# Optimization experiments

Hardware: AMD Instinct MI355X
Metric: run time of the kernel (lower is better)

The kernel has to match this reference:

```python
import jax, jax.numpy as jnp
import numpy as np

N = 16384
D_IN = 128
D_OUT = 128
BETA = 1.0


def setup_inputs() -> dict:
    key = jax.random.key(0)
    k1, k2, k3 = jax.random.split(key, 3)
    x = jax.random.normal(k1, (N, D_IN), dtype=jnp.float32)
    adj = jax.random.uniform(k2, (N, N), dtype=jnp.float32)
    # single-layer MLP (mlp_layers=1 -> channels=[in_dim, out_dim] -> one Linear)
    W_mlp = jax.random.normal(k3, (D_IN, D_OUT), dtype=jnp.float32) * (1.0 / np.sqrt(D_IN))
    b_mlp = jnp.zeros((D_OUT,), dtype=jnp.float32)
    return {"x": x, "adj": adj, "W_mlp": W_mlp, "b_mlp": b_mlp}


def reference(x, adj, W_mlp, b_mlp):
    # softmax aggregator: attention = softmax(adj * beta, axis=-1); x = attention @ x
    attention = jax.nn.softmax(adj * BETA, axis=-1)  # [N, N]
    h = jnp.matmul(attention, x)                      # [N, D_IN]
    # MLP with a single linear layer
    out = jnp.matmul(h, W_mlp) + b_mlp                # [N, D_OUT]
    return out
```

## Files before the change

### kernel.cpp

```cpp
#include <hip/hip_runtime.h>
#include <hip/hip_bf16.h>


typedef short  short8  __attribute__((ext_vector_type(8)));
typedef short  short4v __attribute__((ext_vector_type(4)));
typedef float  floatx4 __attribute__((ext_vector_type(4)));

#define NN 16384
#define DD 128

__device__ __forceinline__ short f2bf(float f) {
    unsigned u = __float_as_uint(f);
    u += 0x7fff + ((u >> 16) & 1);
    return (short)(u >> 16);
}

__global__ __launch_bounds__(256, 2) void xw_kernel(
    const float* __restrict__ x, const float* __restrict__ W, short* __restrict__ yT)
{
    __shared__ short WT[128 * 136];
    const int t  = threadIdx.x;
    const int j0 = blockIdx.x * 64;

    #pragma unroll
    for (int i = 0; i < 16; ++i) {
        int f4 = t + 256 * i;
        int d = f4 >> 5, c4 = f4 & 31;
        float4 v = ((const float4*)W)[f4];
        WT[(4*c4 + 0) * 136 + d] = f2bf(v.x);
        WT[(4*c4 + 1) * 136 + d] = f2bf(v.y);
        WT[(4*c4 + 2) * 136 + d] = f2bf(v.z);
        WT[(4*c4 + 3) * 136 + d] = f2bf(v.w);
    }
    __syncthreads();

    const int lane = t & 63, w = t >> 6;
    const int nl = lane & 15, q = lane >> 4;
    const int j = j0 + 16 * w + nl;
    const float* xrow = x + (size_t)j * DD + 8 * q;

    floatx4 acc[8];
    #pragma unroll
    for (int kt = 0; kt < 8; ++kt) acc[kt] = (floatx4){0.f, 0.f, 0.f, 0.f};

    #pragma unroll
    for (int dstep = 0; dstep < 4; ++dstep) {
        float4 v0 = *(const float4*)(xrow + 32 * dstep);
        float4 v1 = *(const float4*)(xrow + 32 * dstep + 4);
        short8 bf;
        bf[0] = f2bf(v0.x); bf[1] = f2bf(v0.y); bf[2] = f2bf(v0.z); bf[3] = f2bf(v0.w);
        bf[4] = f2bf(v1.x); bf[5] = f2bf(v1.y); bf[6] = f2bf(v1.z); bf[7] = f2bf(v1.w);
        #pragma unroll
        for (int kt = 0; kt < 8; ++kt) {
            short8 af = *(const short8*)(&WT[(16*kt + nl) * 136 + 32*dstep + 8*q]);
            acc[kt] = __builtin_amdgcn_mfma_f32_16x16x32_bf16(af, bf, acc[kt], 0, 0, 0);
        }
    }
    #pragma unroll
    for (int kt = 0; kt < 8; ++kt) {
        #pragma unroll
        for (int r = 0; r < 4; ++r)
            yT[(size_t)(16*kt + 4*q + r) * NN + j] = f2bf(acc[kt][r]);
    }
}

__global__ __launch_bounds__(256, 1) void attn_kernel(
    const float* __restrict__ adj, const short* __restrict__ yT,
    const float* __restrict__ bias, float* __restrict__ out)
{
    __shared__ short A_lds[64 * 136];
    __shared__ short B_lds[128 * 136];
    __shared__ float rs[64];

    const int t  = threadIdx.x;
    const int i0 = blockIdx.x * 64;

    const int cg = t & 31, rg = t >> 5;
    const float* aptr = adj + (size_t)(i0 + rg) * NN + 4 * cg;
    const int bn = t >> 1, bh = t & 1;
    const short* bptr = yT + (size_t)bn * NN + 64 * bh;

    float4 pa[8];
    uint4  pb[8];
    float  psum[8];
    floatx4 acc[8];
    #pragma unroll
    for (int p = 0; p < 8; ++p) psum[p] = 0.f;
    #pragma unroll
    for (int n = 0; n < 8; ++n) acc[n] = (floatx4){0.f, 0.f, 0.f, 0.f};

    const int lane = t & 63, w = t >> 6;
    const int m = lane & 15, q = lane >> 4;
    const short* Arow = &A_lds[(16*w + m) * 136];

    auto load_tile = [&](int kb) {
        #pragma unroll
        for (int p = 0; p < 8; ++p)
            pa[p] = *(const float4*)(aptr + (size_t)(8 * p) * NN + kb);
        #pragma unroll
        for (int jj = 0; jj < 8; ++jj)
            pb[jj] = *(const uint4*)(bptr + kb + 8 * jj);
    };
    auto store_tile = [&]() {
        #pragma unroll
        for (int p = 0; p < 8; ++p) {
            float e0 = __expf(pa[p].x), e1 = __expf(pa[p].y);
            float e2 = __expf(pa[p].z), e3 = __expf(pa[p].w);
            psum[p] += (e0 + e1) + (e2 + e3);
            short4v v; v[0] = f2bf(e0); v[1] = f2bf(e1); v[2] = f2bf(e2); v[3] = f2bf(e3);
            *(short4v*)&A_lds[(rg + 8*p) * 136 + 4*cg] = v;
        }
        #pragma unroll
        for (int jj = 0; jj < 8; ++jj)
            *(uint4*)&B_lds[bn * 136 + 64*bh + 8*jj] = pb[jj];
    };
    auto mma_tile = [&]() {
        #pragma unroll
        for (int ks = 0; ks < 4; ++ks) {
            short8 af = *(const short8*)(Arow + 32*ks + 8*q);
            #pragma unroll
            for (int nt = 0; nt < 8; ++nt) {
                short8 bf = *(const short8*)(&B_lds[(16*nt + m) * 136 + 32*ks + 8*q]);
                acc[nt] = __builtin_amdgcn_mfma_f32_16x16x32_bf16(af, bf, acc[nt], 0, 0, 0);
            }
        }
    };

    load_tile(0);
    store_tile();
    __syncthreads();
    for (int it = 1; it < NN / 128; ++it) {
        load_tile(it * 128);
        mma_tile();
        __syncthreads();
        store_tile();
        __syncthreads();
    }
    mma_tile();

    #pragma unroll
    for (int p = 0; p < 8; ++p) {
        float v = psum[p];
        v += __shfl_xor(v, 1);
        v += __shfl_xor(v, 2);
        v += __shfl_xor(v, 4);
        v += __shfl_xor(v, 8);
        v += __shfl_xor(v, 16);
        if (cg == 0) rs[rg + 8*p] = v;
    }
    __syncthreads();

    float inv[4];
    #pragma unroll
    for (int r = 0; r < 4; ++r) inv[r] = 1.0f / rs[16*w + 4*q + r];
    #pragma unroll
    for (int nt = 0; nt < 8; ++nt) {
        float bv = bias[16*nt + m];
        #pragma unroll
        for (int r = 0; r < 4; ++r)
            out[(size_t)(i0 + 16*w + 4*q + r) * DD + 16*nt + m] = acc[nt][r] * inv[r] + bv;
    }
}

extern "C" void kernel_launch(void* const* d_in, const int* in_sizes, int n_in,
                              void* d_out, int out_size, void* d_ws, size_t ws_size,
                              hipStream_t stream)
{
    const float* x    = (const float*)d_in[0];
    const float* adj  = (const float*)d_in[1];
    const float* W    = (const float*)d_in[2];
    const float* bias = (const float*)d_in[3];
    float* out = (float*)d_out;
    short* yT  = (short*)d_ws;

    hipLaunchKernelGGL(xw_kernel,   dim3(256), dim3(256), 0, stream, x, W, yT);
    hipLaunchKernelGGL(attn_kernel, dim3(256), dim3(256), 0, stream, adj, yT, bias, out);
}
```

Baseline: 1.856 ms.

## Load MFMA operands directly from global into registers, dropping LDS staging

The attention kernel no longer stages the exp(adj) tile and the yT tile through shared memory. Each wave now loads its own 16 rows of adj and all of yT straight into registers in MFMA fragment layout, and double-buffers the loads across two register slots, so all __syncthreads barriers go away. Row sums are reduced with lane shuffles. The trade-off is that every wave re-reads the full yT from global/L2, four times per block instead of once, and the loads are scattered 16-byte accesses, not coalesced tile loads.

```diff
diff --git a/kernel.cpp b/kernel.cpp
--- a/kernel.cpp
+++ b/kernel.cpp
@@ -3,7 +3,6 @@
 
 
 typedef short  short8  __attribute__((ext_vector_type(8)));
-typedef short  short4v __attribute__((ext_vector_type(4)));
 typedef float  floatx4 __attribute__((ext_vector_type(4)));
 
 #define NN 16384
@@ -68,97 +67,69 @@
     const float* __restrict__ adj, const short* __restrict__ yT,
     const float* __restrict__ bias, float* __restrict__ out)
 {
-    __shared__ short A_lds[64 * 136];
-    __shared__ short B_lds[128 * 136];
-    __shared__ float rs[64];
+    const int t  = threadIdx.x;
+    const int la = t & 63, w = t >> 6;
+    const int m = la & 15, q = la >> 4;
+    const int i0 = blockIdx.x * 64 + 16 * w;
 
-    const int t  = threadIdx.x;
-    const int i0 = blockIdx.x * 64;
+    const float* aptr = adj + (size_t)(i0 + m) * NN + 8 * q;
+    const short* bptr = yT + (size_t)m * NN + 8 * q;
 
-    const int cg = t & 31, rg = t >> 5;
-    const float* aptr = adj + (size_t)(i0 + rg) * NN + 4 * cg;
-    const int bn = t >> 1, bh = t & 1;
-    const short* bptr = yT + (size_t)bn * NN + 64 * bh;
-
-    float4 pa[8];
-    uint4  pb[8];
-    float  psum[8];
     floatx4 acc[8];
     #pragma unroll
-    for (int p = 0; p < 8; ++p) psum[p] = 0.f;
-    #pragma unroll
-    for (int n = 0; n < 8; ++n) acc[n] = (floatx4){0.f, 0.f, 0.f, 0.f};
+    for (int nt = 0; nt < 8; ++nt) acc[nt] = (floatx4){0.f, 0.f, 0.f, 0.f};
+    float psumA = 0.f, psumB = 0.f;
 
-    const int lane = t & 63, w = t >> 6;
-    const int m = lane & 15, q = lane >> 4;
-    const short* Arow = &A_lds[(16*w + m) * 136];
+    float4 A00, A01, A10, A11;
+    uint4  B0[8], B1[8];
 
-    auto load_tile = [&](int kb) {
+    auto load_slot = [&](int s, float4& Aa, float4& Ab, uint4* B) {
+        const float* ap = aptr + (size_t)s * 32;
+        Aa = *(const float4*)ap;
+        Ab = *(const float4*)(ap + 4);
+        const short* bp = bptr + (size_t)s * 32;
         #pragma unroll
-        for (int p = 0; p < 8; ++p)
-            pa[p] = *(const float4*)(aptr + (size_t)(8 * p) * NN + kb);
+        for (int nt = 0; nt < 8; ++nt)
+            B[nt] = *(const uint4*)(bp + (size_t)nt * (16 * NN));
+    };
+    auto step = [&](const float4& Aa, const float4& Ab, const uint4* B, float& psum) {
+        float e0 = __expf(Aa.x), e1 = __expf(Aa.y), e2 = __expf(Aa.z), e3 = __expf(Aa.w);
+        float e4 = __expf(Ab.x), e5 = __expf(Ab.y), e6 = __expf(Ab.z), e7 = __expf(Ab.w);
+        psum += ((e0 + e1) + (e2 + e3)) + ((e4 + e5) + (e6 + e7));
+        short8 af;
+        af[0] = f2bf(e0); af[1] = f2bf(e1); af[2] = f2bf(e2); af[3] = f2bf(e3);
+        af[4] = f2bf(e4); af[5] = f2bf(e5); af[6] = f2bf(e6); af[7] = f2bf(e7);
         #pragma unroll
-        for (int jj = 0; jj < 8; ++jj)
-            pb[jj] = *(const uint4*)(bptr + kb + 8 * jj);
-    };
-    auto store_tile = [&]() {
-        #pragma unroll
-        for (int p = 0; p < 8; ++p) {
-            float e0 = __expf(pa[p].x), e1 = __expf(pa[p].y);
-            float e2 = __expf(pa[p].z), e3 = __expf(pa[p].w);
-            psum[p] += (e0 + e1) + (e2 + e3);
-            short4v v; v[0] = f2bf(e0); v[1] = f2bf(e1); v[2] = f2bf(e2); v[3] = f2bf(e3);
-            *(short4v*)&A_lds[(rg + 8*p) * 136 + 4*cg] = v;
-        }
-        #pragma unroll
-        for (int jj = 0; jj < 8; ++jj)
-            *(uint4*)&B_lds[bn * 136 + 64*bh + 8*jj] = pb[jj];
-    };
-    auto mma_tile = [&]() {
-        #pragma unroll
-        for (int ks = 0; ks < 4; ++ks) {
-            short8 af = *(const short8*)(Arow + 32*ks + 8*q);
-            #pragma unroll
-            for (int nt = 0; nt < 8; ++nt) {
-                short8 bf = *(const short8*)(&B_lds[(16*nt + m) * 136 + 32*ks + 8*q]);
-                acc[nt] = __builtin_amdgcn_mfma_f32_16x16x32_bf16(af, bf, acc[nt], 0, 0, 0);
-            }
+        for (int nt = 0; nt < 8; ++nt) {
+            short8 bf = *(const short8*)&B[nt];
+            acc[nt] = __builtin_amdgcn_mfma_f32_16x16x32_bf16(af, bf, acc[nt], 0, 0, 0);
         }
     };
 
-    load_tile(0);
-    store_tile();
-    __syncthreads();
-    for (int it = 1; it < NN / 128; ++it) {
-        load_tile(it * 128);
-        mma_tile();
-        __syncthreads();
-        store_tile();
-        __syncthreads();
+    load_slot(0, A00, A01, B0);
+    load_slot(1, A10, A11, B1);
+    #pragma unroll 1
+    for (int s = 0; s < NN / 32; s += 2) {
+        step(A00, A01, B0, psumA);
+        if (s + 2 < NN / 32) load_slot(s + 2, A00, A01, B0);
+        step(A10, A11, B1, psumB);
+        if (s + 3 < NN / 32) load_slot(s + 3, A10, A11, B1);
     }
-    mma_tile();
+
+    float sum = psumA + psumB;
+    sum += __shfl_xor(sum, 16);
+    sum += __shfl_xor(sum, 32);
+    float inv = 1.0f / sum;
+    float invr[4];
+    #pragma unroll
+    for (int r = 0; r < 4; ++r) invr[r] = __shfl(inv, 4 * q + r);
 
     #pragma unroll
-    for (int p = 0; p < 8; ++p) {
-        float v = psum[p];
-        v += __shfl_xor(v, 1);
-        v += __shfl_xor(v, 2);
-        v += __shfl_xor(v, 4);
-        v += __shfl_xor(v, 8);
-        v += __shfl_xor(v, 16);
-        if (cg == 0) rs[rg + 8*p] = v;
-    }
-    __syncthreads();
-
-    float inv[4];
-    #pragma unroll
-    for (int r = 0; r < 4; ++r) inv[r] = 1.0f / rs[16*w + 4*q + r];
-    #pragma unroll
     for (int nt = 0; nt < 8; ++nt) {
-        float bv = bias[16*nt + m];
+        float bv = bias[16 * nt + m];
         #pragma unroll
         for (int r = 0; r < 4; ++r)
-            out[(size_t)(i0 + 16*w + 4*q + r) * DD + 16*nt + m] = acc[nt][r] * inv[r] + bv;
+            out[(size_t)(i0 + 4 * q + r) * DD + 16 * nt + m] = acc[nt][r] * invr[r] + bv;
     }
 }
 
```

New measurement: 1.763 ms. 5.0% less time.
